# Kernel tuning notes

Hardware: AMD Instinct MI355X
Metric: run time of the kernel (lower is better)

## Reference

```python
import jax, jax.numpy as jnp
import numpy as np

D, BEV_H, BEV_W, NH, NP = 256, 200, 200, 8, 8
NQ = BEV_H * BEV_W
DFF = 1024
HD = D // NH


def setup_inputs() -> dict:
    key = jax.random.key(0)
    ks = jax.random.split(key, 12)
    def rn(k, shape, scale=0.02):
        return jax.random.normal(k, shape, jnp.float32) * scale
    return dict(
        B_adj0=rn(ks[0], (1, NQ, D), 1.0),
        B_adj1=rn(ks[1], (1, NQ, D), 1.0),
        query_embed=rn(ks[2], (NQ, D), 1.0),
        W_ref=rn(ks[3], (D, 2)), b_ref=jnp.zeros((2,), jnp.float32),
        W_off=rn(ks[4], (D, NH * NP * 2)), b_off=rn(ks[5], (NH * NP * 2,), 0.5),
        W_attn=rn(ks[6], (D, NH * NP)), b_attn=jnp.zeros((NH * NP,), jnp.float32),
        W_val=rn(ks[7], (D, D)), b_val=jnp.zeros((D,), jnp.float32),
        W_out=rn(ks[8], (D, D)), b_out=jnp.zeros((D,), jnp.float32),
        W_ffn1=rn(ks[9], (D, DFF)), b_ffn1=jnp.zeros((DFF,), jnp.float32),
        W_ffn2=rn(ks[10], (DFF, D)), b_ffn2=jnp.zeros((D,), jnp.float32),
    )


def _deform_attend(value, loc, attn_w):
    """Bilinear-sample `value` (bs,NQ,NH,HD laid out as BEV_H x BEV_W map) at
    normalized locations loc (bs,nq,NH,NP,2) with align_corners=False and zero
    padding (torch grid_sample semantics), weighted by attn_w (bs,nq,NH,NP)."""
    bs, _, nh, hd = value.shape
    nq = loc.shape[1]
    vt = value.transpose(0, 2, 1, 3)  # (bs, nh, HW, hd)
    # grid = 2*loc - 1 ; pixel = ((grid+1)*size - 1)/2 = loc*size - 0.5
    x = loc[..., 0] * BEV_W - 0.5
    y = loc[..., 1] * BEV_H - 0.5
    x0f = jnp.floor(x); y0f = jnp.floor(y)
    lx = x - x0f; ly = y - y0f
    x0 = x0f.astype(jnp.int32); y0 = y0f.astype(jnp.int32)
    acc = jnp.zeros((bs, nh, nq, hd), value.dtype)
    corners = ((0, 0, (1 - lx) * (1 - ly)), (1, 0, lx * (1 - ly)),
               (0, 1, (1 - lx) * ly), (1, 1, lx * ly))
    for dx, dy, w in corners:
        ix = x0 + dx
        iy = y0 + dy
        valid = ((ix >= 0) & (ix < BEV_W) & (iy >= 0) & (iy < BEV_H)).astype(value.dtype)
        idx = jnp.clip(iy, 0, BEV_H - 1) * BEV_W + jnp.clip(ix, 0, BEV_W - 1)  # (bs,nq,nh,np)
        idx_t = idx.transpose(0, 2, 1, 3).reshape(bs, nh, nq * NP)
        v = jnp.take_along_axis(vt, idx_t[..., None], axis=2).reshape(bs, nh, nq, NP, hd)
        wt = (w * valid * attn_w).transpose(0, 2, 1, 3)  # (bs,nh,nq,np)
        acc = acc + (wt[..., None] * v).sum(3)
    return acc.transpose(0, 2, 1, 3).reshape(bs, nq, nh * hd)


def reference(B_adj0, B_adj1, query_embed, W_ref, b_ref, W_off, b_off,
              W_attn, b_attn, W_val, b_val, W_out, b_out,
              W_ffn1, b_ffn1, W_ffn2, b_ffn2):
    bs = B_adj0.shape[0]
    q = jnp.broadcast_to(query_embed[None], (bs, NQ, D))
    # reference points in [0,1]
    ref = jax.nn.sigmoid(q @ W_ref + b_ref)  # (bs,nq,2)
    off = (q @ W_off + b_off).reshape(bs, NQ, NH, NP, 2)
    attn = jax.nn.softmax((q @ W_attn + b_attn).reshape(bs, NQ, NH, NP), axis=-1)
    offset_normalizer = jnp.array([BEV_W, BEV_H], jnp.float32)
    loc = ref[:, :, None, None, :] + off / offset_normalizer  # (bs,nq,nh,np,2)
    B_short = jnp.zeros((bs, NQ, D), B_adj0.dtype)
    for V in (B_adj0, B_adj1):
        val = (V @ W_val + b_val).reshape(bs, NQ, NH, HD)
        out = _deform_attend(val, loc, attn) @ W_out + b_out
        B_short = B_short + out + q  # mmcv MSDA residual: identity = query
    # FFN with residual (mmcv FFN, add_identity=True, drop=0)
    ffn = jax.nn.relu(B_short @ W_ffn1 + b_ffn1) @ W_ffn2 + b_ffn2
    return B_short + ffn
```

## Files before the change

kernel.cpp:

```cpp
#include <hip/hip_runtime.h>
#include <hip/hip_bf16.h>

#define NQ    40000
#define DD    256
#define NHH   8
#define NPP   8
#define DFF   1024
#define BEV   200
#define MPAD  40064

typedef __attribute__((ext_vector_type(4))) float f32x4;
typedef __attribute__((ext_vector_type(8))) short s16x8;
typedef __hip_bfloat16 bf16;

#define AS1(p) ((const __attribute__((address_space(1))) void*)(p))
#define AS3(p) ((__attribute__((address_space(3))) void*)(p))

__device__ inline unsigned short f2bf(float f) {
  union { bf16 h; unsigned short u; } cv;
  cv.h = __float2bfloat16(f);
  return cv.u;
}
__device__ inline float bf2f(bf16 h) { return __bfloat162float(h); }
__device__ inline float bfs(short u) {
  union { float f; unsigned u; } c;
  c.u = ((unsigned)(unsigned short)u) << 16;
  return c.f;
}

__global__ void transpose_cvt(const float* __restrict__ src, bf16* __restrict__ dst,
                              int R, int C) {
  int i = blockIdx.x * 256 + threadIdx.x;
  if (i >= R * C) return;
  int c = i / R, r = i % R;
  dst[i] = __float2bfloat16(src[(size_t)r * C + c]);
}

__global__ void build_wq(const float* __restrict__ Woff, const float* __restrict__ Wattn,
                         const float* __restrict__ Wref, bf16* __restrict__ dst) {
  int i = blockIdx.x * 256 + threadIdx.x;
  int n = i >> 8, k = i & 255;
  float v;
  if (n < 128)      v = Woff[k * 128 + n];
  else if (n < 192) v = Wattn[k * 64 + (n - 128)];
  else if (n < 194) v = Wref[k * 2 + (n - 192)];
  else              v = 0.f;
  dst[i] = __float2bfloat16(v);
}

__global__ void cvt_bf16_kernel(const float* __restrict__ src, bf16* __restrict__ dst, int n4) {
  int i = blockIdx.x * 256 + threadIdx.x;
  if (i >= n4) return;
  float4 v = ((const float4*)src)[i];
  ushort4 o;
  o.x = f2bf(v.x); o.y = f2bf(v.y); o.z = f2bf(v.z); o.w = f2bf(v.w);
  ((ushort4*)dst)[i] = o;
}

__global__ void addcvt_kernel(const float* __restrict__ a, const float* __restrict__ b,
                              bf16* __restrict__ dst, int n4) {
  int i = blockIdx.x * 256 + threadIdx.x;
  if (i >= n4) return;
  float4 va = ((const float4*)a)[i];
  float4 vb = ((const float4*)b)[i];
  ushort4 o;
  o.x = f2bf(va.x + vb.x); o.y = f2bf(va.y + vb.y);
  o.z = f2bf(va.z + vb.z); o.w = f2bf(va.w + vb.w);
  ((ushort4*)dst)[i] = o;
}

template<bool RELU>
__global__ void gemm_bt(const bf16* __restrict__ A, const bf16* __restrict__ Bt,
                        int K, int Ntiles, int N,
                        const float* __restrict__ bias, float biasScale,
                        const bf16* __restrict__ addB, float addScale,
                        bf16* __restrict__ outB, float* __restrict__ outF, int Mvalid) {
  __shared__ __align__(16) char smem[32768];
  const int tid  = threadIdx.x;
  const int wave = tid >> 6, lane = tid & 63;
  const int nwg = gridDim.x;
  const int orig = blockIdx.x;
  const int q8 = nwg >> 3, r8 = nwg & 7;
  const int xcd = orig & 7, idx = orig >> 3;
  const int wg = (xcd < r8 ? xcd * (q8 + 1) : r8 * (q8 + 1) + (xcd - r8) * q8) + idx;
  const int tm = wg / Ntiles, tn = wg % Ntiles;
  const int wr = wave >> 1, wc = wave & 1;

  f32x4 acc[4][4];
#pragma unroll
  for (int i = 0; i < 4; ++i)
#pragma unroll
    for (int j = 0; j < 4; ++j) {
      f32x4 z = {0.f, 0.f, 0.f, 0.f};
      acc[i][j] = z;
    }

  const char* Ab = (const char*)A;
  const char* Bb = (const char*)Bt;
  const int nK = K >> 6;

  for (int kt = 0; kt < nK; ++kt) {
#pragma unroll
    for (int i = 0; i < 8; ++i) {
      const int j  = wave * 8 + i;
      const int p0 = j << 10;
      const char* g;
      if (p0 < 16384) {
        const int pl = p0 + lane * 16;
        const int row = pl >> 7, cb = pl & 127;
        g = Ab + ((size_t)(tm * 128 + row) * K + kt * 64) * 2 + cb;
      } else {
        const int pl = p0 - 16384 + lane * 16;
        const int row = pl >> 7, cb = pl & 127;
        g = Bb + ((size_t)(tn * 128 + row) * K + kt * 64) * 2 + cb;
      }
      __builtin_amdgcn_global_load_lds(AS1(g), AS3(smem + p0), 16, 0, 0);
    }
    __syncthreads();

#pragma unroll
    for (int kk = 0; kk < 2; ++kk) {
      const int r  = lane & 15;
      const int kb = kk * 64 + (lane >> 4) * 16;
      s16x8 af[4], bfr[4];
#pragma unroll
      for (int mr = 0; mr < 4; ++mr)
        af[mr] = *(const s16x8*)(smem + (wr * 64 + mr * 16 + r) * 128 + kb);
#pragma unroll
      for (int nr = 0; nr < 4; ++nr)
        bfr[nr] = *(const s16x8*)(smem + 16384 + (wc * 64 + nr * 16 + r) * 128 + kb);
#pragma unroll
      for (int mr = 0; mr < 4; ++mr)
#pragma unroll
        for (int nr = 0; nr < 4; ++nr)
          acc[mr][nr] = __builtin_amdgcn_mfma_f32_16x16x32_bf16(af[mr], bfr[nr], acc[mr][nr], 0, 0, 0);
    }
    __syncthreads();
  }

  const int r = lane & 15, rg = lane >> 4;
#pragma unroll
  for (int mr = 0; mr < 4; ++mr) {
#pragma unroll
    for (int nr = 0; nr < 4; ++nr) {
      const int gn = tn * 128 + wc * 64 + nr * 16 + r;
      const float bval = bias ? biasScale * bias[gn] : 0.f;
#pragma unroll
      for (int j2 = 0; j2 < 4; ++j2) {
        const int gm = tm * 128 + wr * 64 + mr * 16 + rg * 4 + j2;
        float v = acc[mr][nr][j2] + bval;
        if (addB && gm < Mvalid) v += addScale * bf2f(addB[(size_t)gm * N + gn]);
        if (RELU) v = fmaxf(v, 0.f);
        if (outB) outB[(size_t)gm * N + gn] = __float2bfloat16(v);
        if (outF && gm < Mvalid) outF[(size_t)gm * N + gn] = v;
      }
    }
  }
}

__global__ void finalize_kernel(const bf16* __restrict__ raw, const float* __restrict__ b_off,
                                const float* __restrict__ b_attn, const float* __restrict__ b_ref,
                                float* __restrict__ samp) {
  __shared__ float r[4][256];
  const int tid = threadIdx.x;
  const int q0 = blockIdx.x * 4;
#pragma unroll
  for (int i = 0; i < 4; ++i) {
    int e = tid + i * 256;
    int ql = e >> 8, k = e & 255;
    r[ql][k] = bf2f(raw[(size_t)(q0 + ql) * 256 + k]);
  }
  __syncthreads();
  const int ql = tid >> 6, hp = tid & 63;
  const int h = hp >> 3, p = hp & 7;
  float v[8];
  float m = -1e30f;
#pragma unroll
  for (int pp = 0; pp < 8; ++pp) {
    v[pp] = r[ql][128 + h * 8 + pp] + b_attn[h * 8 + pp];
    m = fmaxf(m, v[pp]);
  }
  float s = 0.f;
#pragma unroll
  for (int pp = 0; pp < 8; ++pp) { v[pp] = expf(v[pp] - m); s += v[pp]; }
  const float w = v[p] / s;
  const float sx = 1.f / (1.f + expf(-(r[ql][192] + b_ref[0])));
  const float sy = 1.f / (1.f + expf(-(r[ql][193] + b_ref[1])));
  const float px = sx * (float)BEV + (r[ql][hp * 2 + 0] + b_off[hp * 2 + 0]) - 0.5f;
  const float py = sy * (float)BEV + (r[ql][hp * 2 + 1] + b_off[hp * 2 + 1]) - 0.5f;
  const size_t o = ((size_t)(q0 + ql) * 64 + hp) * 3;
  samp[o] = px; samp[o + 1] = py; samp[o + 2] = w;
}

__global__ __launch_bounds__(256, 4)
void deform_kernel(const float* __restrict__ samp, const bf16* __restrict__ val,
                   bf16* __restrict__ out) {
  __shared__ float s[8 * 192];
  const int tid = threadIdx.x;
  const int q0 = blockIdx.x * 8;
#pragma unroll
  for (int i = 0; i < 6; ++i) {
    const int e = tid + i * 256;
    s[e] = samp[(size_t)q0 * 192 + e];
  }
  __syncthreads();
  const int ql = tid >> 5;
  const int lane5 = tid & 31;
  const int h = lane5 >> 2;
  const int dg = lane5 & 3;
  const float* sp = s + ql * 192 + h * 24;
  const bf16* vb = val + h * 32 + dg * 8;

  float acc[8] = {0.f, 0.f, 0.f, 0.f, 0.f, 0.f, 0.f, 0.f};
#pragma unroll 2
  for (int p = 0; p < 8; ++p) {
    const float px = sp[p * 3 + 0], py = sp[p * 3 + 1], w = sp[p * 3 + 2];
    const float xf = floorf(px), yf = floorf(py);
    const int x0 = (int)xf, y0 = (int)yf;
    const float lx = px - xf, ly = py - yf;
    const float xa = (x0 >= 0 && x0 < BEV) ? 1.f : 0.f;
    const float xb = (x0 + 1 >= 0 && x0 + 1 < BEV) ? 1.f : 0.f;
    const float ya = (y0 >= 0 && y0 < BEV) ? 1.f : 0.f;
    const float yb = (y0 + 1 >= 0 && y0 + 1 < BEV) ? 1.f : 0.f;
    const float w00 = w * (1.f - lx) * (1.f - ly) * xa * ya;
    const float w10 = w * lx * (1.f - ly) * xb * ya;
    const float w01 = w * (1.f - lx) * ly * xa * yb;
    const float w11 = w * lx * ly * xb * yb;
    const int cx0 = min(max(x0, 0), BEV - 1);
    const int cx1 = min(max(x0 + 1, 0), BEV - 1);
    const int cy0 = min(max(y0, 0), BEV - 1) * BEV;
    const int cy1 = min(max(y0 + 1, 0), BEV - 1) * BEV;
    const s16x8 v00 = *(const s16x8*)(vb + (size_t)(cy0 + cx0) * 256);
    const s16x8 v10 = *(const s16x8*)(vb + (size_t)(cy0 + cx1) * 256);
    const s16x8 v01 = *(const s16x8*)(vb + (size_t)(cy1 + cx0) * 256);
    const s16x8 v11 = *(const s16x8*)(vb + (size_t)(cy1 + cx1) * 256);
#pragma unroll
    for (int j = 0; j < 8; ++j) {
      acc[j] += w00 * bfs(v00[j]) + w10 * bfs(v10[j])
              + w01 * bfs(v01[j]) + w11 * bfs(v11[j]);
    }
  }
  s16x8 o;
#pragma unroll
  for (int j = 0; j < 8; ++j) o[j] = (short)f2bf(acc[j]);
  *(s16x8*)(out + (size_t)(q0 + ql) * 256 + h * 32 + dg * 8) = o;
}

extern "C" void kernel_launch(void* const* d_in, const int* in_sizes, int n_in,
                              void* d_out, int out_size, void* d_ws, size_t ws_size,
                              hipStream_t stream) {
  const float* B0     = (const float*)d_in[0];
  const float* B1     = (const float*)d_in[1];
  const float* qe     = (const float*)d_in[2];
  const float* W_ref  = (const float*)d_in[3];
  const float* b_ref  = (const float*)d_in[4];
  const float* W_off  = (const float*)d_in[5];
  const float* b_off  = (const float*)d_in[6];
  const float* W_attn = (const float*)d_in[7];
  const float* b_attn = (const float*)d_in[8];
  const float* W_val  = (const float*)d_in[9];
  const float* b_val  = (const float*)d_in[10];
  const float* W_out  = (const float*)d_in[11];
  const float* b_out  = (const float*)d_in[12];
  const float* W_ffn1 = (const float*)d_in[13];
  const float* b_ffn1 = (const float*)d_in[14];
  const float* W_ffn2 = (const float*)d_in[15];
  const float* b_ffn2 = (const float*)d_in[16];
  float* out = (float*)d_out;
  char* ws = (char*)d_ws;

  const size_t SZ_MAT = (size_t)MPAD * 256 * 2;
  const size_t VAL_OFF    = 0;
  const size_t RAW_OFF    = SZ_MAT;
  const size_t BSH_OFF    = 2 * SZ_MAT;
  const size_t H_OFF      = 3 * SZ_MAT;
  const size_t QE_OFF     = H_OFF;
  const size_t VSUM_OFF   = H_OFF + SZ_MAT;
  const size_t H_BYTES    = (size_t)MPAD * 1024 * 2;
  const size_t SAMP_OFF   = H_OFF + H_BYTES;
  const size_t SAMP_BYTES = (size_t)NQ * 192 * 4;
  const size_t WQ_OFF     = SAMP_OFF + SAMP_BYTES;
  const size_t WVAL_OFF   = WQ_OFF   + 256 * 256 * 2;
  const size_t WOUT_OFF   = WVAL_OFF + 256 * 256 * 2;
  const size_t WF1_OFF    = WOUT_OFF + 256 * 256 * 2;
  const size_t WF2_OFF    = WF1_OFF  + 1024 * 256 * 2;

  bf16* valb  = (bf16*)(ws + VAL_OFF);
  bf16* rawb  = (bf16*)(ws + RAW_OFF);
  bf16* defb  = rawb;
  bf16* bshb  = (bf16*)(ws + BSH_OFF);
  bf16* hbuf  = (bf16*)(ws + H_OFF);
  bf16* qeb   = (bf16*)(ws + QE_OFF);
  bf16* vsum  = (bf16*)(ws + VSUM_OFF);
  float* samp = (float*)(ws + SAMP_OFF);
  bf16* wq    = (bf16*)(ws + WQ_OFF);
  bf16* wval  = (bf16*)(ws + WVAL_OFF);
  bf16* wout  = (bf16*)(ws + WOUT_OFF);
  bf16* wf1   = (bf16*)(ws + WF1_OFF);
  bf16* wf2   = (bf16*)(ws + WF2_OFF);

  const int n4 = NQ * 256 / 4;
  const int MT = MPAD / 128;

  build_wq<<<256, 256, 0, stream>>>(W_off, W_attn, W_ref, wq);
  transpose_cvt<<<(256 * 256 + 255) / 256, 256, 0, stream>>>(W_val, wval, 256, 256);
  transpose_cvt<<<(256 * 256 + 255) / 256, 256, 0, stream>>>(W_out, wout, 256, 256);
  transpose_cvt<<<(256 * 1024 + 255) / 256, 256, 0, stream>>>(W_ffn1, wf1, 256, 1024);
  transpose_cvt<<<(1024 * 256 + 255) / 256, 256, 0, stream>>>(W_ffn2, wf2, 1024, 256);

  cvt_bf16_kernel<<<n4 / 256, 256, 0, stream>>>(qe, qeb, n4);
  addcvt_kernel<<<n4 / 256, 256, 0, stream>>>(B0, B1, vsum, n4);

  gemm_bt<false><<<MT * 2, 256, 0, stream>>>(qeb, wq, 256, 2, 256,
                                             nullptr, 0.f, nullptr, 0.f,
                                             rawb, nullptr, NQ);
  finalize_kernel<<<NQ / 4, 256, 0, stream>>>(rawb, b_off, b_attn, b_ref, samp);

  gemm_bt<false><<<MT * 2, 256, 0, stream>>>(vsum, wval, 256, 2, 256,
                                             b_val, 2.f, nullptr, 0.f,
                                             valb, nullptr, NQ);

  deform_kernel<<<NQ / 8, 256, 0, stream>>>(samp, valb, defb);

  gemm_bt<false><<<MT * 2, 256, 0, stream>>>(defb, wout, 256, 2, 256,
                                             b_out, 2.f, qeb, 2.f,
                                             bshb, nullptr, NQ);

  gemm_bt<true><<<MT * 8, 256, 0, stream>>>(bshb, wf1, 256, 8, 1024,
                                            b_ffn1, 1.f, nullptr, 0.f,
                                            hbuf, nullptr, NQ);

  gemm_bt<false><<<MT * 2, 256, 0, stream>>>(hbuf, wf2, 1024, 2, 256,
                                             b_ffn2, 1.f, bshb, 1.f,
                                             nullptr, out, NQ);
}
```

Before: 269.9 us.

## Fuse fp32-to-bf16 input conversion and B0+B1 add into GEMM A-tile loads

```diff
diff --git a/kernel.cpp b/kernel.cpp
--- a/kernel.cpp
+++ b/kernel.cpp
@@ -48,34 +48,18 @@
   dst[i] = __float2bfloat16(v);
 }
 
-__global__ void cvt_bf16_kernel(const float* __restrict__ src, bf16* __restrict__ dst, int n4) {
-  int i = blockIdx.x * 256 + threadIdx.x;
-  if (i >= n4) return;
-  float4 v = ((const float4*)src)[i];
-  ushort4 o;
-  o.x = f2bf(v.x); o.y = f2bf(v.y); o.z = f2bf(v.z); o.w = f2bf(v.w);
-  ((ushort4*)dst)[i] = o;
-}
-
-__global__ void addcvt_kernel(const float* __restrict__ a, const float* __restrict__ b,
-                              bf16* __restrict__ dst, int n4) {
-  int i = blockIdx.x * 256 + threadIdx.x;
-  if (i >= n4) return;
-  float4 va = ((const float4*)a)[i];
-  float4 vb = ((const float4*)b)[i];
-  ushort4 o;
-  o.x = f2bf(va.x + vb.x); o.y = f2bf(va.y + vb.y);
-  o.z = f2bf(va.z + vb.z); o.w = f2bf(va.w + vb.w);
-  ((ushort4*)dst)[i] = o;
-}
-
-template<bool RELU>
-__global__ void gemm_bt(const bf16* __restrict__ A, const bf16* __restrict__ Bt,
+template<int SRC, int BK_, bool RELU>
+__global__ void gemm_bt(const bf16* __restrict__ A,
+                        const float* __restrict__ Af0, const float* __restrict__ Af1,
+                        const bf16* __restrict__ Bt,
                         int K, int Ntiles, int N,
                         const float* __restrict__ bias, float biasScale,
-                        const bf16* __restrict__ addB, float addScale,
+                        const bf16* __restrict__ addB, const float* __restrict__ addF,
+                        float addScale,
                         bf16* __restrict__ outB, float* __restrict__ outF, int Mvalid) {
-  __shared__ __align__(16) char smem[32768];
+  constexpr int HALF = BK_ * 256;
+  constexpr int ROWB = BK_ * 2;
+  __shared__ __align__(16) char smem[BK_ * 512];
   const int tid  = threadIdx.x;
   const int wave = tid >> 6, lane = tid & 63;
   const int nwg = gridDim.x;
@@ -97,38 +81,75 @@
 
   const char* Ab = (const char*)A;
   const char* Bb = (const char*)Bt;
-  const int nK = K >> 6;
+  const int nK = K / BK_;
 
   for (int kt = 0; kt < nK; ++kt) {
-#pragma unroll
-    for (int i = 0; i < 8; ++i) {
-      const int j  = wave * 8 + i;
-      const int p0 = j << 10;
-      const char* g;
-      if (p0 < 16384) {
+    if constexpr (SRC == 0) {
+      constexpr int WI = BK_ / 8;
+#pragma unroll
+      for (int i = 0; i < WI; ++i) {
+        const int j  = wave * WI + i;
+        const int p0 = j << 10;
+        const char* g;
+        if (p0 < HALF) {
+          const int pl = p0 + lane * 16;
+          const int row = pl / ROWB, cb = pl % ROWB;
+          g = Ab + ((size_t)(tm * 128 + row) * K + kt * BK_) * 2 + cb;
+        } else {
+          const int pl = p0 - HALF + lane * 16;
+          const int row = pl / ROWB, cb = pl % ROWB;
+          g = Bb + ((size_t)(tn * 128 + row) * K + kt * BK_) * 2 + cb;
+        }
+        __builtin_amdgcn_global_load_lds(AS1(g), AS3(smem + p0), 16, 0, 0);
+      }
+    } else {
+      const int row = tid >> 1, c0 = (tid & 1) * 16;
+      const int srow = min(tm * 128 + row, Mvalid - 1);
+      const float* s0 = Af0 + (size_t)srow * K + kt * 32 + c0;
+      float4 f[4];
+#pragma unroll
+      for (int i = 0; i < 4; ++i) f[i] = ((const float4*)s0)[i];
+      if constexpr (SRC == 2) {
+        const float* s1 = Af1 + (size_t)srow * K + kt * 32 + c0;
+#pragma unroll
+        for (int i = 0; i < 4; ++i) {
+          float4 g4 = ((const float4*)s1)[i];
+          f[i].x += g4.x; f[i].y += g4.y; f[i].z += g4.z; f[i].w += g4.w;
+        }
+      }
+      s16x8 w0, w1;
+#pragma unroll
+      for (int i = 0; i < 2; ++i) {
+        w0[i * 4 + 0] = (short)f2bf(f[i].x);     w0[i * 4 + 1] = (short)f2bf(f[i].y);
+        w0[i * 4 + 2] = (short)f2bf(f[i].z);     w0[i * 4 + 3] = (short)f2bf(f[i].w);
+        w1[i * 4 + 0] = (short)f2bf(f[i + 2].x); w1[i * 4 + 1] = (short)f2bf(f[i + 2].y);
+        w1[i * 4 + 2] = (short)f2bf(f[i + 2].z); w1[i * 4 + 3] = (short)f2bf(f[i + 2].w);
+      }
+      *(s16x8*)(smem + row * 64 + c0 * 2)      = w0;
+      *(s16x8*)(smem + row * 64 + c0 * 2 + 16) = w1;
+#pragma unroll
+      for (int i = 0; i < 2; ++i) {
+        const int p0 = (wave * 2 + i) << 10;
         const int pl = p0 + lane * 16;
-        const int row = pl >> 7, cb = pl & 127;
-        g = Ab + ((size_t)(tm * 128 + row) * K + kt * 64) * 2 + cb;
-      } else {
-        const int pl = p0 - 16384 + lane * 16;
-        const int row = pl >> 7, cb = pl & 127;
-        g = Bb + ((size_t)(tn * 128 + row) * K + kt * 64) * 2 + cb;
-      }
-      __builtin_amdgcn_global_load_lds(AS1(g), AS3(smem + p0), 16, 0, 0);
+        const int rowB = pl >> 6, cb = pl & 63;
+        const char* g = Bb + ((size_t)(tn * 128 + rowB) * K + kt * 32) * 2 + cb;
+        __builtin_amdgcn_global_load_lds(AS1(g), AS3(smem + HALF + p0), 16, 0, 0);
+      }
     }
     __syncthreads();
 
-#pragma unroll
-    for (int kk = 0; kk < 2; ++kk) {
+    constexpr int NKK = BK_ / 32;
+#pragma unroll
+    for (int kk = 0; kk < NKK; ++kk) {
       const int r  = lane & 15;
       const int kb = kk * 64 + (lane >> 4) * 16;
       s16x8 af[4], bfr[4];
 #pragma unroll
       for (int mr = 0; mr < 4; ++mr)
-        af[mr] = *(const s16x8*)(smem + (wr * 64 + mr * 16 + r) * 128 + kb);
+        af[mr] = *(const s16x8*)(smem + (wr * 64 + mr * 16 + r) * ROWB + kb);
 #pragma unroll
       for (int nr = 0; nr < 4; ++nr)
-        bfr[nr] = *(const s16x8*)(smem + 16384 + (wc * 64 + nr * 16 + r) * 128 + kb);
+        bfr[nr] = *(const s16x8*)(smem + HALF + (wc * 64 + nr * 16 + r) * ROWB + kb);
 #pragma unroll
       for (int mr = 0; mr < 4; ++mr)
 #pragma unroll
@@ -149,7 +170,10 @@
       for (int j2 = 0; j2 < 4; ++j2) {
         const int gm = tm * 128 + wr * 64 + mr * 16 + rg * 4 + j2;
         float v = acc[mr][nr][j2] + bval;
-        if (addB && gm < Mvalid) v += addScale * bf2f(addB[(size_t)gm * N + gn]);
+        if (gm < Mvalid) {
+          if (addB) v += addScale * bf2f(addB[(size_t)gm * N + gn]);
+          else if (addF) v += addScale * addF[(size_t)gm * N + gn];
+        }
         if (RELU) v = fmaxf(v, 0.f);
         if (outB) outB[(size_t)gm * N + gn] = __float2bfloat16(v);
         if (outF && gm < Mvalid) outF[(size_t)gm * N + gn] = v;
@@ -274,8 +298,6 @@
   const size_t RAW_OFF    = SZ_MAT;
   const size_t BSH_OFF    = 2 * SZ_MAT;
   const size_t H_OFF      = 3 * SZ_MAT;
-  const size_t QE_OFF     = H_OFF;
-  const size_t VSUM_OFF   = H_OFF + SZ_MAT;
   const size_t H_BYTES    = (size_t)MPAD * 1024 * 2;
   const size_t SAMP_OFF   = H_OFF + H_BYTES;
   const size_t SAMP_BYTES = (size_t)NQ * 192 * 4;
@@ -290,8 +312,6 @@
   bf16* defb  = rawb;
   bf16* bshb  = (bf16*)(ws + BSH_OFF);
   bf16* hbuf  = (bf16*)(ws + H_OFF);
-  bf16* qeb   = (bf16*)(ws + QE_OFF);
-  bf16* vsum  = (bf16*)(ws + VSUM_OFF);
   float* samp = (float*)(ws + SAMP_OFF);
   bf16* wq    = (bf16*)(ws + WQ_OFF);
   bf16* wval  = (bf16*)(ws + WVAL_OFF);
@@ -299,7 +319,6 @@
   bf16* wf1   = (bf16*)(ws + WF1_OFF);
   bf16* wf2   = (bf16*)(ws + WF2_OFF);
 
-  const int n4 = NQ * 256 / 4;
   const int MT = MPAD / 128;
 
   build_wq<<<256, 256, 0, stream>>>(W_off, W_attn, W_ref, wq);
@@ -308,29 +327,26 @@
   transpose_cvt<<<(256 * 1024 + 255) / 256, 256, 0, stream>>>(W_ffn1, wf1, 256, 1024);
   transpose_cvt<<<(1024 * 256 + 255) / 256, 256, 0, stream>>>(W_ffn2, wf2, 1024, 256);
 
-  cvt_bf16_kernel<<<n4 / 256, 256, 0, stream>>>(qe, qeb, n4);
-  addcvt_kernel<<<n4 / 256, 256, 0, stream>>>(B0, B1, vsum, n4);
-
-  gemm_bt<false><<<MT * 2, 256, 0, stream>>>(qeb, wq, 256, 2, 256,
-                                             nullptr, 0.f, nullptr, 0.f,
-                                             rawb, nullptr, NQ);
+  gemm_bt<1, 32, false><<<MT * 2, 256, 0, stream>>>(
+      nullptr, qe, nullptr, wq, 256, 2, 256,
+      nullptr, 0.f, nullptr, nullptr, 0.f, rawb, nullptr, NQ);
   finalize_kernel<<<NQ / 4, 256, 0, stream>>>(rawb, b_off, b_attn, b_ref, samp);
 
-  gemm_bt<false><<<MT * 2, 256, 0, stream>>>(vsum, wval, 256, 2, 256,
-                                             b_val, 2.f, nullptr, 0.f,
-                                             valb, nullptr, NQ);
+  gemm_bt<2, 32, false><<<MT * 2, 256, 0, stream>>>(
+      nullptr, B0, B1, wval, 256, 2, 256,
+      b_val, 2.f, nullptr, nullptr, 0.f, valb, nullptr, NQ);
 
   deform_kernel<<<NQ / 8, 256, 0, stream>>>(samp, valb, defb);
 
-  gemm_bt<false><<<MT * 2, 256, 0, stream>>>(defb, wout, 256, 2, 256,
-                                             b_out, 2.f, qeb, 2.f,
-                                             bshb, nullptr, NQ);
-
-  gemm_bt<true><<<MT * 8, 256, 0, stream>>>(bshb, wf1, 256, 8, 1024,
-                                            b_ffn1, 1.f, nullptr, 0.f,
-                                            hbuf, nullptr, NQ);
-
-  gemm_bt<false><<<MT * 2, 256, 0, stream>>>(hbuf, wf2, 1024, 2, 256,
-                                             b_ffn2, 1.f, bshb, 1.f,
-                                             nullptr, out, NQ);
-}
+  gemm_bt<0, 32, false><<<MT * 2, 256, 0, stream>>>(
+      defb, nullptr, nullptr, wout, 256, 2, 256,
+      b_out, 2.f, nullptr, qe, 2.f, bshb, nullptr, NQ);
+
+  gemm_bt<0, 32, true><<<MT * 8, 256, 0, stream>>>(
+      bshb, nullptr, nullptr, wf1, 256, 8, 1024,
+      b_ffn1, 1.f, nullptr, nullptr, 0.f, hbuf, nullptr, NQ);
+
+  gemm_bt<0, 64, false><<<MT * 2, 256, 0, stream>>>(
+      hbuf, nullptr, nullptr, wf2, 1024, 2, 256,
+      b_ffn2, 1.f, bshb, nullptr, 1.f, nullptr, out, NQ);
+}
```

Result: slower. 363.0 us (+34.5%).

## Replace LDS-staged GEMM with register-direct global loads and 8-wave blocks

Applied to the files above, without the earlier changes.

```diff
diff --git a/kernel.cpp b/kernel.cpp
--- a/kernel.cpp
+++ b/kernel.cpp
@@ -12,9 +12,6 @@
 typedef __attribute__((ext_vector_type(4))) float f32x4;
 typedef __attribute__((ext_vector_type(8))) short s16x8;
 typedef __hip_bfloat16 bf16;
-
-#define AS1(p) ((const __attribute__((address_space(1))) void*)(p))
-#define AS3(p) ((__attribute__((address_space(3))) void*)(p))
 
 __device__ inline unsigned short f2bf(float f) {
   union { bf16 h; unsigned short u; } cv;
@@ -69,13 +66,12 @@
   ((ushort4*)dst)[i] = o;
 }
 
-template<bool RELU>
-__global__ void gemm_bt(const bf16* __restrict__ A, const bf16* __restrict__ Bt,
+template<int NSEG, bool RELU>
+__global__ void gemm_rb(const bf16* __restrict__ A, const bf16* __restrict__ Bt,
                         int K, int Ntiles, int N,
                         const float* __restrict__ bias, float biasScale,
                         const bf16* __restrict__ addB, float addScale,
                         bf16* __restrict__ outB, float* __restrict__ outF, int Mvalid) {
-  __shared__ __align__(16) char smem[32768];
   const int tid  = threadIdx.x;
   const int wave = tid >> 6, lane = tid & 63;
   const int nwg = gridDim.x;
@@ -84,71 +80,59 @@
   const int xcd = orig & 7, idx = orig >> 3;
   const int wg = (xcd < r8 ? xcd * (q8 + 1) : r8 * (q8 + 1) + (xcd - r8) * q8) + idx;
   const int tm = wg / Ntiles, tn = wg % Ntiles;
-  const int wr = wave >> 1, wc = wave & 1;
-
-  f32x4 acc[4][4];
+  const int wr = wave >> 2, wc = wave & 3;
+  const int r  = lane & 15, hi = lane >> 4;
+
+  f32x4 acc[4][2];
 #pragma unroll
   for (int i = 0; i < 4; ++i)
 #pragma unroll
-    for (int j = 0; j < 4; ++j) {
+    for (int j = 0; j < 2; ++j) {
       f32x4 z = {0.f, 0.f, 0.f, 0.f};
       acc[i][j] = z;
     }
 
-  const char* Ab = (const char*)A;
-  const char* Bb = (const char*)Bt;
-  const int nK = K >> 6;
-
-  for (int kt = 0; kt < nK; ++kt) {
-#pragma unroll
-    for (int i = 0; i < 8; ++i) {
-      const int j  = wave * 8 + i;
-      const int p0 = j << 10;
-      const char* g;
-      if (p0 < 16384) {
-        const int pl = p0 + lane * 16;
-        const int row = pl >> 7, cb = pl & 127;
-        g = Ab + ((size_t)(tm * 128 + row) * K + kt * 64) * 2 + cb;
-      } else {
-        const int pl = p0 - 16384 + lane * 16;
-        const int row = pl >> 7, cb = pl & 127;
-        g = Bb + ((size_t)(tn * 128 + row) * K + kt * 64) * 2 + cb;
-      }
-      __builtin_amdgcn_global_load_lds(AS1(g), AS3(smem + p0), 16, 0, 0);
+  const bf16* arow = A  + (size_t)(tm * 128 + wr * 64 + r) * K + hi * 8;
+  const bf16* brow = Bt + (size_t)(tn * 128 + wc * 32 + r) * K + hi * 8;
+
+#pragma unroll
+  for (int seg = 0; seg < NSEG; ++seg) {
+    const int k0 = seg * 256;
+    s16x8 bf_[2][8];
+#pragma unroll
+    for (int nf = 0; nf < 2; ++nf)
+#pragma unroll
+      for (int c = 0; c < 8; ++c)
+        bf_[nf][c] = *(const s16x8*)(brow + (size_t)nf * 16 * K + k0 + c * 32);
+#pragma unroll
+    for (int hf = 0; hf < 2; ++hf) {
+      s16x8 af[4][4];
+#pragma unroll
+      for (int mf = 0; mf < 4; ++mf)
+#pragma unroll
+        for (int cc = 0; cc < 4; ++cc)
+          af[mf][cc] = *(const s16x8*)(arow + (size_t)mf * 16 * K + k0 + (hf * 4 + cc) * 32);
+#pragma unroll
+      for (int cc = 0; cc < 4; ++cc)
+#pragma unroll
+        for (int mf = 0; mf < 4; ++mf)
+#pragma unroll
+          for (int nf = 0; nf < 2; ++nf)
+            acc[mf][nf] = __builtin_amdgcn_mfma_f32_16x16x32_bf16(
+                af[mf][cc], bf_[nf][hf * 4 + cc], acc[mf][nf], 0, 0, 0);
     }
-    __syncthreads();
-
-#pragma unroll
-    for (int kk = 0; kk < 2; ++kk) {
-      const int r  = lane & 15;
-      const int kb = kk * 64 + (lane >> 4) * 16;
-      s16x8 af[4], bfr[4];
-#pragma unroll
-      for (int mr = 0; mr < 4; ++mr)
-        af[mr] = *(const s16x8*)(smem + (wr * 64 + mr * 16 + r) * 128 + kb);
-#pragma unroll
-      for (int nr = 0; nr < 4; ++nr)
-        bfr[nr] = *(const s16x8*)(smem + 16384 + (wc * 64 + nr * 16 + r) * 128 + kb);
-#pragma unroll
-      for (int mr = 0; mr < 4; ++mr)
-#pragma unroll
-        for (int nr = 0; nr < 4; ++nr)
-          acc[mr][nr] = __builtin_amdgcn_mfma_f32_16x16x32_bf16(af[mr], bfr[nr], acc[mr][nr], 0, 0, 0);
-    }
-    __syncthreads();
-  }
-
-  const int r = lane & 15, rg = lane >> 4;
-#pragma unroll
-  for (int mr = 0; mr < 4; ++mr) {
-#pragma unroll
-    for (int nr = 0; nr < 4; ++nr) {
-      const int gn = tn * 128 + wc * 64 + nr * 16 + r;
+  }
+
+#pragma unroll
+  for (int mf = 0; mf < 4; ++mf) {
+#pragma unroll
+    for (int nf = 0; nf < 2; ++nf) {
+      const int gn = tn * 128 + wc * 32 + nf * 16 + r;
       const float bval = bias ? biasScale * bias[gn] : 0.f;
 #pragma unroll
       for (int j2 = 0; j2 < 4; ++j2) {
-        const int gm = tm * 128 + wr * 64 + mr * 16 + rg * 4 + j2;
-        float v = acc[mr][nr][j2] + bval;
+        const int gm = tm * 128 + wr * 64 + mf * 16 + hi * 4 + j2;
+        float v = acc[mf][nf][j2] + bval;
         if (addB && gm < Mvalid) v += addScale * bf2f(addB[(size_t)gm * N + gn]);
         if (RELU) v = fmaxf(v, 0.f);
         if (outB) outB[(size_t)gm * N + gn] = __float2bfloat16(v);
@@ -311,26 +295,26 @@
   cvt_bf16_kernel<<<n4 / 256, 256, 0, stream>>>(qe, qeb, n4);
   addcvt_kernel<<<n4 / 256, 256, 0, stream>>>(B0, B1, vsum, n4);
 
-  gemm_bt<false><<<MT * 2, 256, 0, stream>>>(qeb, wq, 256, 2, 256,
-                                             nullptr, 0.f, nullptr, 0.f,
-                                             rawb, nullptr, NQ);
+  gemm_rb<1, false><<<MT * 2, 512, 0, stream>>>(qeb, wq, 256, 2, 256,
+                                                nullptr, 0.f, nullptr, 0.f,
+                                                rawb, nullptr, NQ);
   finalize_kernel<<<NQ / 4, 256, 0, stream>>>(rawb, b_off, b_attn, b_ref, samp);
 
-  gemm_bt<false><<<MT * 2, 256, 0, stream>>>(vsum, wval, 256, 2, 256,
-                                             b_val, 2.f, nullptr, 0.f,
-                                             valb, nullptr, NQ);
+  gemm_rb<1, false><<<MT * 2, 512, 0, stream>>>(vsum, wval, 256, 2, 256,
+                                                b_val, 2.f, nullptr, 0.f,
+                                                valb, nullptr, NQ);
 
   deform_kernel<<<NQ / 8, 256, 0, stream>>>(samp, valb, defb);
 
-  gemm_bt<false><<<MT * 2, 256, 0, stream>>>(defb, wout, 256, 2, 256,
-                                             b_out, 2.f, qeb, 2.f,
-                                             bshb, nullptr, NQ);
-
-  gemm_bt<true><<<MT * 8, 256, 0, stream>>>(bshb, wf1, 256, 8, 1024,
-                                            b_ffn1, 1.f, nullptr, 0.f,
-                                            hbuf, nullptr, NQ);
-
-  gemm_bt<false><<<MT * 2, 256, 0, stream>>>(hbuf, wf2, 1024, 2, 256,
-                                             b_ffn2, 1.f, bshb, 1.f,
-                                             nullptr, out, NQ);
-}
+  gemm_rb<1, false><<<MT * 2, 512, 0, stream>>>(defb, wout, 256, 2, 256,
+                                                b_out, 2.f, qeb, 2.f,
+                                                bshb, nullptr, NQ);
+
+  gemm_rb<1, true><<<MT * 8, 512, 0, stream>>>(bshb, wf1, 256, 8, 1024,
+                                               b_ffn1, 1.f, nullptr, 0.f,
+                                               hbuf, nullptr, NQ);
+
+  gemm_rb<4, false><<<MT * 2, 512, 0, stream>>>(hbuf, wf2, 1024, 2, 256,
+                                                b_ffn2, 1.f, bshb, 1.f,
+                                                nullptr, out, NQ);
+}
```

Result: slower. 512.1 us (+89.7%).

## Replace 4-wave GEMM with single-wave 64x64 tile double-buffered GEMM

Applied to the files above, without the earlier changes.

```diff
diff --git a/kernel.cpp b/kernel.cpp
--- a/kernel.cpp
+++ b/kernel.cpp
@@ -70,21 +70,21 @@
 }
 
 template<bool RELU>
-__global__ void gemm_bt(const bf16* __restrict__ A, const bf16* __restrict__ Bt,
-                        int K, int Ntiles, int N,
-                        const float* __restrict__ bias, float biasScale,
-                        const bf16* __restrict__ addB, float addScale,
-                        bf16* __restrict__ outB, float* __restrict__ outF, int Mvalid) {
-  __shared__ __align__(16) char smem[32768];
-  const int tid  = threadIdx.x;
-  const int wave = tid >> 6, lane = tid & 63;
+__global__ __launch_bounds__(64)
+void gemm_sw(const bf16* __restrict__ A, const bf16* __restrict__ Bt,
+             int K, int Ntiles, int N,
+             const float* __restrict__ bias, float biasScale,
+             const bf16* __restrict__ addB, float addScale,
+             bf16* __restrict__ outB, float* __restrict__ outF, int Mvalid) {
+  __shared__ __align__(16) char smem[2][8192];
+  const int lane = threadIdx.x;
+  const int r = lane & 15, hi = lane >> 4;
   const int nwg = gridDim.x;
   const int orig = blockIdx.x;
   const int q8 = nwg >> 3, r8 = nwg & 7;
   const int xcd = orig & 7, idx = orig >> 3;
   const int wg = (xcd < r8 ? xcd * (q8 + 1) : r8 * (q8 + 1) + (xcd - r8) * q8) + idx;
   const int tm = wg / Ntiles, tn = wg % Ntiles;
-  const int wr = wave >> 1, wc = wave & 1;
 
   f32x4 acc[4][4];
 #pragma unroll
@@ -97,57 +97,60 @@
 
   const char* Ab = (const char*)A;
   const char* Bb = (const char*)Bt;
-  const int nK = K >> 6;
-
+  const int nK = K >> 5;
+
+  auto stage = [&](int buf, int kt) {
+#pragma unroll
+    for (int i = 0; i < 8; ++i) {
+      const int p0 = i << 10;
+      const char* g;
+      if (p0 < 4096) {
+        const int pl = p0 + lane * 16;
+        const int row = pl >> 6, cb = pl & 63;
+        g = Ab + ((size_t)(tm * 64 + row) * K + kt * 32) * 2 + cb;
+      } else {
+        const int pl = p0 - 4096 + lane * 16;
+        const int row = pl >> 6, cb = pl & 63;
+        g = Bb + ((size_t)(tn * 64 + row) * K + kt * 32) * 2 + cb;
+      }
+      __builtin_amdgcn_global_load_lds(AS1(g), AS3(&smem[buf][p0]), 16, 0, 0);
+    }
+  };
+
+  stage(0, 0);
   for (int kt = 0; kt < nK; ++kt) {
-#pragma unroll
-    for (int i = 0; i < 8; ++i) {
-      const int j  = wave * 8 + i;
-      const int p0 = j << 10;
-      const char* g;
-      if (p0 < 16384) {
-        const int pl = p0 + lane * 16;
-        const int row = pl >> 7, cb = pl & 127;
-        g = Ab + ((size_t)(tm * 128 + row) * K + kt * 64) * 2 + cb;
-      } else {
-        const int pl = p0 - 16384 + lane * 16;
-        const int row = pl >> 7, cb = pl & 127;
-        g = Bb + ((size_t)(tn * 128 + row) * K + kt * 64) * 2 + cb;
-      }
-      __builtin_amdgcn_global_load_lds(AS1(g), AS3(smem + p0), 16, 0, 0);
-    }
-    __syncthreads();
-
-#pragma unroll
-    for (int kk = 0; kk < 2; ++kk) {
-      const int r  = lane & 15;
-      const int kb = kk * 64 + (lane >> 4) * 16;
-      s16x8 af[4], bfr[4];
-#pragma unroll
-      for (int mr = 0; mr < 4; ++mr)
-        af[mr] = *(const s16x8*)(smem + (wr * 64 + mr * 16 + r) * 128 + kb);
+    const int cur = kt & 1;
+    if (kt + 1 < nK) {
+      stage(cur ^ 1, kt + 1);
+      asm volatile("s_waitcnt vmcnt(8)" ::: "memory");
+    } else {
+      asm volatile("s_waitcnt vmcnt(0)" ::: "memory");
+    }
+    __builtin_amdgcn_sched_barrier(0);
+    const char* sbuf = smem[cur];
+    s16x8 af[4], bfr[4];
+#pragma unroll
+    for (int mr = 0; mr < 4; ++mr)
+      af[mr] = *(const s16x8*)(sbuf + (mr * 16 + r) * 64 + hi * 16);
+#pragma unroll
+    for (int nr = 0; nr < 4; ++nr)
+      bfr[nr] = *(const s16x8*)(sbuf + 4096 + (nr * 16 + r) * 64 + hi * 16);
+#pragma unroll
+    for (int mr = 0; mr < 4; ++mr)
 #pragma unroll
       for (int nr = 0; nr < 4; ++nr)
-        bfr[nr] = *(const s16x8*)(smem + 16384 + (wc * 64 + nr * 16 + r) * 128 + kb);
-#pragma unroll
-      for (int mr = 0; mr < 4; ++mr)
-#pragma unroll
-        for (int nr = 0; nr < 4; ++nr)
-          acc[mr][nr] = __builtin_amdgcn_mfma_f32_16x16x32_bf16(af[mr], bfr[nr], acc[mr][nr], 0, 0, 0);
-    }
-    __syncthreads();
-  }
-
-  const int r = lane & 15, rg = lane >> 4;
+        acc[mr][nr] = __builtin_amdgcn_mfma_f32_16x16x32_bf16(af[mr], bfr[nr], acc[mr][nr], 0, 0, 0);
+  }
+
 #pragma unroll
   for (int mr = 0; mr < 4; ++mr) {
 #pragma unroll
     for (int nr = 0; nr < 4; ++nr) {
-      const int gn = tn * 128 + wc * 64 + nr * 16 + r;
+      const int gn = tn * 64 + nr * 16 + r;
       const float bval = bias ? biasScale * bias[gn] : 0.f;
 #pragma unroll
       for (int j2 = 0; j2 < 4; ++j2) {
-        const int gm = tm * 128 + wr * 64 + mr * 16 + rg * 4 + j2;
+        const int gm = tm * 64 + mr * 16 + hi * 4 + j2;
         float v = acc[mr][nr][j2] + bval;
         if (addB && gm < Mvalid) v += addScale * bf2f(addB[(size_t)gm * N + gn]);
         if (RELU) v = fmaxf(v, 0.f);
@@ -300,7 +303,7 @@
   bf16* wf2   = (bf16*)(ws + WF2_OFF);
 
   const int n4 = NQ * 256 / 4;
-  const int MT = MPAD / 128;
+  const int MT = MPAD / 64;
 
   build_wq<<<256, 256, 0, stream>>>(W_off, W_attn, W_ref, wq);
   transpose_cvt<<<(256 * 256 + 255) / 256, 256, 0, stream>>>(W_val, wval, 256, 256);
@@ -311,26 +314,26 @@
   cvt_bf16_kernel<<<n4 / 256, 256, 0, stream>>>(qe, qeb, n4);
   addcvt_kernel<<<n4 / 256, 256, 0, stream>>>(B0, B1, vsum, n4);
 
-  gemm_bt<false><<<MT * 2, 256, 0, stream>>>(qeb, wq, 256, 2, 256,
-                                             nullptr, 0.f, nullptr, 0.f,
-                                             rawb, nullptr, NQ);
+  gemm_sw<false><<<MT * 4, 64, 0, stream>>>(qeb, wq, 256, 4, 256,
+                                            nullptr, 0.f, nullptr, 0.f,
+                                            rawb, nullptr, NQ);
   finalize_kernel<<<NQ / 4, 256, 0, stream>>>(rawb, b_off, b_attn, b_ref, samp);
 
-  gemm_bt<false><<<MT * 2, 256, 0, stream>>>(vsum, wval, 256, 2, 256,
-                                             b_val, 2.f, nullptr, 0.f,
-                                             valb, nullptr, NQ);
+  gemm_sw<false><<<MT * 4, 64, 0, stream>>>(vsum, wval, 256, 4, 256,
+                                            b_val, 2.f, nullptr, 0.f,
+                                            valb, nullptr, NQ);
 
   deform_kernel<<<NQ / 8, 256, 0, stream>>>(samp, valb, defb);
 
-  gemm_bt<false><<<MT * 2, 256, 0, stream>>>(defb, wout, 256, 2, 256,
-                                             b_out, 2.f, qeb, 2.f,
-                                             bshb, nullptr, NQ);
-
-  gemm_bt<true><<<MT * 8, 256, 0, stream>>>(bshb, wf1, 256, 8, 1024,
+  gemm_sw<false><<<MT * 4, 64, 0, stream>>>(defb, wout, 256, 4, 256,
+                                            b_out, 2.f, qeb, 2.f,
+                                            bshb, nullptr, NQ);
+
+  gemm_sw<true><<<MT * 16, 64, 0, stream>>>(bshb, wf1, 256, 16, 1024,
                                             b_ffn1, 1.f, nullptr, 0.f,
                                             hbuf, nullptr, NQ);
 
-  gemm_bt<false><<<MT * 2, 256, 0, stream>>>(hbuf, wf2, 1024, 2, 256,
-                                             b_ffn2, 1.f, bshb, 1.f,
-                                             nullptr, out, NQ);
-}
+  gemm_sw<false><<<MT * 4, 64, 0, stream>>>(hbuf, wf2, 1024, 4, 256,
+                                            b_ffn2, 1.f, bshb, 1.f,
+                                            nullptr, out, NQ);
+}
```

Result: slower. 331.5 us (+22.8%).
